# Performance work log

Hardware: AMD Instinct MI355X
Metric: run time of the kernel (lower is better)

## Reference

```python
import jax, jax.numpy as jnp
import numpy as np

BN_INV = 1.0 / np.sqrt(1.0 + 1e-5)  # eval-mode BatchNorm1d with running_mean=0, running_var=1


def _lin_bn_relu(x, W, g, b):
    # Linear(no bias) -> BN(eval) -> ReLU
    return jax.nn.relu((x @ W.T) * (g * BN_INV) + b)


def setup_inputs() -> dict:
    key = jax.random.key(0)
    ks = jax.random.split(key, 24)
    B, P, N, C, H, OUT = 8, 1024, 20, 32, 256, 256
    s = 0.05
    inp = {
        "polylines": jax.random.normal(ks[0], (B, P, N, C), dtype=jnp.float32),
        "polylines_mask": jax.random.randint(ks[1], (B, P, N), 0, 2) > 0,
        # pre_mlps: [Lin(C->H,no bias)+BN+ReLU] x2, Lin(H->H, bias)
        "pre_w0": jax.random.normal(ks[2], (H, C), dtype=jnp.float32) * s,
        "pre_g0": jnp.ones((H,), jnp.float32),
        "pre_b0": jnp.zeros((H,), jnp.float32),
        "pre_w1": jax.random.normal(ks[3], (H, H), dtype=jnp.float32) * s,
        "pre_g1": jnp.ones((H,), jnp.float32),
        "pre_b1": jnp.zeros((H,), jnp.float32),
        "pre_w2": jax.random.normal(ks[4], (H, H), dtype=jnp.float32) * s,
        "pre_bias2": jnp.zeros((H,), jnp.float32),
        # mlps: c_in=2H -> [H,H,H]
        "mlp_w0": jax.random.normal(ks[5], (H, 2 * H), dtype=jnp.float32) * s,
        "mlp_g0": jnp.ones((H,), jnp.float32),
        "mlp_b0": jnp.zeros((H,), jnp.float32),
        "mlp_w1": jax.random.normal(ks[6], (H, H), dtype=jnp.float32) * s,
        "mlp_g1": jnp.ones((H,), jnp.float32),
        "mlp_b1": jnp.zeros((H,), jnp.float32),
        "mlp_w2": jax.random.normal(ks[7], (H, H), dtype=jnp.float32) * s,
        "mlp_bias2": jnp.zeros((H,), jnp.float32),
        # out_mlps (without_norm): Lin(H->H,bias)+ReLU, Lin(H->OUT,bias)
        "out_w0": jax.random.normal(ks[8], (H, H), dtype=jnp.float32) * s,
        "out_b0": jnp.zeros((H,), jnp.float32),
        "out_w1": jax.random.normal(ks[9], (OUT, H), dtype=jnp.float32) * s,
        "out_b1": jnp.zeros((OUT,), jnp.float32),
    }
    return inp


def reference(polylines, polylines_mask,
              pre_w0, pre_g0, pre_b0, pre_w1, pre_g1, pre_b1, pre_w2, pre_bias2,
              mlp_w0, mlp_g0, mlp_b0, mlp_w1, mlp_g1, mlp_b1, mlp_w2, mlp_bias2,
              out_w0, out_b0, out_w1, out_b1):
    # gather->MLP->zero-scatter is equivalent to dense MLP followed by mask-zeroing
    # (all per-point ops are elementwise / last-dim matmuls).
    m = polylines_mask[..., None].astype(polylines.dtype)  # (B,P,N,1)

    x = _lin_bn_relu(polylines, pre_w0, pre_g0, pre_b0)
    x = _lin_bn_relu(x, pre_w1, pre_g1, pre_b1)
    x = (x @ pre_w2.T + pre_bias2) * m                      # (B,P,N,H) zero at invalid

    pooled = x.max(axis=2)                                  # (B,P,H) max over zero-filled buffer
    x = jnp.concatenate(
        [x, jnp.broadcast_to(pooled[:, :, None, :], x.shape)], axis=-1)  # (B,P,N,2H)

    x = _lin_bn_relu(x, mlp_w0, mlp_g0, mlp_b0)
    x = _lin_bn_relu(x, mlp_w1, mlp_g1, mlp_b1)
    x = (x @ mlp_w2.T + mlp_bias2) * m                      # (B,P,N,H)

    buf = x.max(axis=2)                                     # (B,P,H)

    valid = jnp.any(polylines_mask, axis=-1)                # sum(mask)>0
    y = jax.nn.relu(buf @ out_w0.T + out_b0)
    y = (y @ out_w1.T + out_b1) * valid[..., None].astype(buf.dtype)  # (B,P,OUT)
    return y
```

## Files before the change

### kernel.cpp

```cpp
#include <hip/hip_runtime.h>
#include <stdint.h>
#include <stddef.h>

typedef __bf16 bf16;
typedef __bf16 bf16x4 __attribute__((ext_vector_type(4)));
typedef __bf16 bf16x8 __attribute__((ext_vector_type(8)));
typedef float f32x4 __attribute__((ext_vector_type(4)));
typedef float f32x16 __attribute__((ext_vector_type(16)));

#define BNI 0.9999950000374996f
#define NROW 240
#define TOTROW 163840
#define NPOLY 8192

#define AADDR(r, ch) ((r)*256 + ((((ch) ^ ((r)&31)))<<3))

#define OFF_ACT 0
#define OFF_WB  122880
#define OFF_T2  155648
#define OFF_VAL 161792
#define LDS_TOTAL 161840

#define WS_PRE_W0 0
#define WS_PRE_W1 8192
#define WS_PRE_W2 73728
#define WS_MLP_W0 139264
#define WS_MLP_W1 270336
#define WS_MLP_W2 335872
#define WS_OUT_W0 401408
#define WS_OUT_W1 466944

__device__ __forceinline__ bf16 f2b(float f){
  unsigned int i = __builtin_bit_cast(unsigned int, f);
  unsigned int r = i + 0x7fffu + ((i >> 16) & 1u);
  unsigned short h = (unsigned short)(r >> 16);
  return __builtin_bit_cast(bf16, h);
}
__device__ __forceinline__ float b2f(bf16 x){
  unsigned short u = __builtin_bit_cast(unsigned short, x);
  union { unsigned int i; float f; } v; v.i = ((unsigned int)u) << 16; return v.f;
}
__device__ __forceinline__ bf16x8 ld8f(const float* p, float sc){
  f32x4 a = *(const f32x4*)p;
  f32x4 b = *(const f32x4*)(p + 4);
  bf16x8 r;
  #pragma unroll
  for (int j = 0; j < 4; ++j){ r[j] = f2b(a[j]*sc); r[4+j] = f2b(b[j]*sc); }
  return r;
}

__global__ __launch_bounds__(256)
void prep_kernel(const float* s0, const float* s1, const float* s2, const float* s3,
                 const float* s4, const float* s5, const float* s6, const float* s7,
                 const float* g0, const float* g1, const float* g3, const float* g4,
                 bf16* dst)
{
  const int offs[8] = {WS_PRE_W0, WS_PRE_W1, WS_PRE_W2, WS_MLP_W0,
                       WS_MLP_W1, WS_MLP_W2, WS_OUT_W0, WS_OUT_W1};
  const int sz[8]   = {8192, 65536, 65536, 131072, 65536, 65536, 65536, 65536};
  const int ld[8]   = {32, 256, 256, 512, 256, 256, 256, 256};
  int r = blockIdx.y;
  const float* src = s0;
  if (r == 1) src = s1; else if (r == 2) src = s2; else if (r == 3) src = s3;
  else if (r == 4) src = s4; else if (r == 5) src = s5; else if (r == 6) src = s6;
  else if (r == 7) src = s7;
  const float* gp = (r==0)?g0:(r==1)?g1:(r==3)?g3:(r==4)?g4:nullptr;
  int i = (blockIdx.x*256 + threadIdx.x)*8;
  if (i < sz[r]){
    float sc = gp ? gp[i/ld[r]]*BNI : 1.0f;
    *(bf16x8*)&dst[offs[r] + i] = ld8f(src + i, sc);
  }
}

__device__ __forceinline__ void stageLoad(bf16x8* v, const bf16* W, int ldK, int c64, int tid){
  #pragma unroll
  for (int i = 0; i < 8; ++i){
    int id = tid + 256*i;
    int fr = id >> 5, kc = id & 31;
    v[i] = *(const bf16x8*)(W + (size_t)(c64*64 + fr)*ldK + kc*8);
  }
}
__device__ __forceinline__ void stageStore(const bf16x8* v, bf16* wbuf, int tid){
  #pragma unroll
  for (int i = 0; i < 8; ++i){
    int id = tid + 256*i;
    int fr = id >> 5, kc = id & 31;
    *(bf16x8*)&wbuf[fr*256 + ((kc ^ (fr & 31))<<3)] = v[i];
  }
}

template<int RELU, int MASK, int ADDT2>
__device__ __forceinline__ void epiT(
    const f32x16& acc, int nt, int row, int poly, float mk, bool valid,
    bf16* sAct, const bf16* sT2, const float* bptr, int hi)
{
  #pragma unroll
  for (int q2 = 0; q2 < 4; ++q2){
    int f0 = nt*32 + 8*q2 + 4*hi;
    f32x4 bb = *(const f32x4*)(bptr + f0);
    bf16x4 tv = {};
    if (ADDT2) tv = *(const bf16x4*)&sT2[poly*256 + f0];
    bf16x4 o;
    #pragma unroll
    for (int j = 0; j < 4; ++j){
      float v = acc[4*q2 + j];
      if (ADDT2) v += b2f(tv[j]);
      v += bb[j];
      if (RELU) v = fmaxf(v, 0.0f);
      if (MASK) v *= mk;
      o[j] = f2b(v);
    }
    if (valid)
      *(bf16x4*)&sAct[row*256 + (((nt*4 + q2) ^ (row & 31))<<3) + 4*hi] = o;
  }
}

template<int RELU, int MASK, int ADDT2>
__device__ __forceinline__ void layerT(
    bf16* sAct, bf16* wbuf, const bf16* sT2,
    const bf16* W, int ldK, const float* bptr,
    const int* maskp, int blk, int w, int lane32, int hi, int tid)
{
  const int row0 = w*64 + lane32, row1 = w*64 + 32 + lane32;
  bf16x8 B0[16], B1[16];
  #pragma unroll
  for (int t = 0; t < 16; ++t){
    B0[t] = *(const bf16x8*)&sAct[AADDR(row0, 2*t + hi)];
    B1[t] = *(const bf16x8*)&sAct[AADDR(row1, 2*t + hi)];
  }
  float mk0 = 1.0f, mk1 = 1.0f;
  if (MASK){
    int g0 = blk*NROW + row0;
    mk0 = (g0 < TOTROW && maskp[g0]) ? 1.0f : 0.0f;
    int g1 = blk*NROW + row1;
    mk1 = (row1 < NROW && g1 < TOTROW && maskp[g1]) ? 1.0f : 0.0f;
  }
  const int poly0 = row0/20;
  const int poly1 = (row1 < NROW ? row1 : 0)/20;

  bf16x8 st[8];
  stageLoad(st, W, ldK, 0, tid);
  __syncthreads();
  stageStore(st, wbuf, tid);
  #pragma unroll 1
  for (int c = 0; c < 4; ++c){
    __syncthreads();
    if (c < 3) stageLoad(st, W, ldK, c + 1, tid);
    #pragma unroll
    for (int h2 = 0; h2 < 2; ++h2){
      int nt = c*2 + h2;
      f32x16 a0 = {}, a1 = {};
      #pragma unroll
      for (int t = 0; t < 16; ++t){
        int fr = h2*32 + lane32;
        bf16x8 wf = *(const bf16x8*)&wbuf[fr*256 + (((2*t + hi) ^ (fr & 31))<<3)];
        a0 = __builtin_amdgcn_mfma_f32_32x32x16_bf16(wf, B0[t], a0, 0, 0, 0);
        a1 = __builtin_amdgcn_mfma_f32_32x32x16_bf16(wf, B1[t], a1, 0, 0, 0);
      }
      epiT<RELU,MASK,ADDT2>(a0, nt, row0, poly0, mk0, true, sAct, sT2, bptr, hi);
      epiT<RELU,MASK,ADDT2>(a1, nt, row1, poly1, mk1, row1 < NROW, sAct, sT2, bptr, hi);
    }
    if (c < 3){ __syncthreads(); stageStore(st, wbuf, tid); }
  }
}

__device__ __forceinline__ void poolT(const bf16* sAct, bf16* sPool, int tid){
  #pragma unroll
  for (int i = 0; i < 2; ++i){
    int id = tid + 256*i;
    if (id < 384){
      int poly = id >> 5, c = id & 31;
      float m[8];
      bf16x8 v0 = *(const bf16x8*)&sAct[AADDR(poly*20, c)];
      #pragma unroll
      for (int j = 0; j < 8; ++j) m[j] = b2f(v0[j]);
      for (int r = 1; r < 20; ++r){
        bf16x8 v = *(const bf16x8*)&sAct[AADDR(poly*20 + r, c)];
        #pragma unroll
        for (int j = 0; j < 8; ++j) m[j] = fmaxf(m[j], b2f(v[j]));
      }
      bf16x8 o;
      #pragma unroll
      for (int j = 0; j < 8; ++j) o[j] = f2b(m[j]);
      *(bf16x8*)&sPool[AADDR(poly, c)] = o;
    }
  }
}

__global__ __launch_bounds__(256, 1)
void traj_kernel(const float* __restrict__ poly, const int* __restrict__ maskp,
                 const float* pre_b0, const float* pre_b1, const float* pre_bias2,
                 const float* mlp_b0, const float* mlp_b1, const float* mlp_bias2,
                 const float* out_b0, const float* out_b1,
                 const bf16* __restrict__ ws,
                 float* __restrict__ outp)
{
  extern __shared__ char smem[];
  bf16*  sAct   = (bf16*)(smem + OFF_ACT);
  bf16*  wbuf   = (bf16*)(smem + OFF_WB);
  bf16*  sPool  = wbuf;
  bf16*  sT2    = (bf16*)(smem + OFF_T2);
  float* sValid = (float*)(smem + OFF_VAL);
  bf16*  sY     = sAct;

  const int tid = threadIdx.x;
  const int w = tid >> 6, L = tid & 63, lane32 = L & 31, hi = L >> 5;
  const int row0 = w*64 + lane32, row1 = w*64 + 32 + lane32;
  const int blk = blockIdx.x;

  const bf16* pw0 = ws + WS_PRE_W0;
  const bf16* pw1 = ws + WS_PRE_W1;
  const bf16* pw2 = ws + WS_PRE_W2;
  const bf16* mw0 = ws + WS_MLP_W0;
  const bf16* mw1 = ws + WS_MLP_W1;
  const bf16* mw2 = ws + WS_MLP_W2;
  const bf16* ow0 = ws + WS_OUT_W0;
  const bf16* ow1 = ws + WS_OUT_W1;

  #pragma unroll
  for (int i = 0; i < 4; ++i){
    int id = tid + 256*i;
    if (id < 960){
      int row = id >> 2, c = id & 3;
      int grow = blk*NROW + row;
      bf16x8 v = {};
      if (grow < TOTROW) v = ld8f(poly + (size_t)grow*32 + c*8, 1.0f);
      *(bf16x8*)&sAct[AADDR(row, c)] = v;
    }
  }
  if (tid < 12){
    float v = 0.0f;
    #pragma unroll
    for (int r = 0; r < 20; ++r){
      int g = blk*NROW + tid*20 + r;
      if (g < TOTROW && maskp[g]) v = 1.0f;
    }
    sValid[tid] = v;
  }
  __syncthreads();

  {
    bf16x8 Bp0[2], Bp1[2];
    #pragma unroll
    for (int t = 0; t < 2; ++t){
      Bp0[t] = *(const bf16x8*)&sAct[AADDR(row0, 2*t + hi)];
      Bp1[t] = *(const bf16x8*)&sAct[AADDR(row1, 2*t + hi)];
    }
    #pragma unroll 1
    for (int nt = 0; nt < 8; ++nt){
      f32x16 a0 = {}, a1 = {};
      #pragma unroll
      for (int t = 0; t < 2; ++t){
        bf16x8 wf = *(const bf16x8*)(pw0 + (size_t)(nt*32 + lane32)*32 + 16*t + 8*hi);
        a0 = __builtin_amdgcn_mfma_f32_32x32x16_bf16(wf, Bp0[t], a0, 0, 0, 0);
        a1 = __builtin_amdgcn_mfma_f32_32x32x16_bf16(wf, Bp1[t], a1, 0, 0, 0);
      }
      epiT<1,0,0>(a0, nt, row0, 0, 1.0f, true, sAct, sT2, pre_b0, hi);
      epiT<1,0,0>(a1, nt, row1, 0, 1.0f, row1 < NROW, sAct, sT2, pre_b0, hi);
    }
  }

  layerT<1,0,0>(sAct, wbuf, sT2, pw1, 256, pre_b1,    maskp, blk, w, lane32, hi, tid);
  layerT<0,1,0>(sAct, wbuf, sT2, pw2, 256, pre_bias2, maskp, blk, w, lane32, hi, tid);

  __syncthreads();
  poolT(sAct, sPool, tid);
  __syncthreads();

  {
    bf16x8 Bp[16];
    #pragma unroll
    for (int t = 0; t < 16; ++t)
      Bp[t] = *(const bf16x8*)&sPool[AADDR(lane32, 2*t + hi)];
    #pragma unroll 1
    for (int m = 0; m < 2; ++m){
      int nt = w*2 + m;
      f32x16 acc = {};
      #pragma unroll
      for (int t = 0; t < 16; ++t){
        bf16x8 wf = *(const bf16x8*)(mw0 + (size_t)(nt*32 + lane32)*512 + 256 + 16*t + 8*hi);
        acc = __builtin_amdgcn_mfma_f32_32x32x16_bf16(wf, Bp[t], acc, 0, 0, 0);
      }
      if (lane32 < 12){
        #pragma unroll
        for (int q2 = 0; q2 < 4; ++q2){
          int f0 = nt*32 + 8*q2 + 4*hi;
          bf16x4 o;
          #pragma unroll
          for (int j = 0; j < 4; ++j) o[j] = f2b(acc[4*q2 + j]);
          *(bf16x4*)&sT2[lane32*256 + f0] = o;
        }
      }
    }
  }
  __syncthreads();

  layerT<1,0,1>(sAct, wbuf, sT2, mw0, 512, mlp_b0,    maskp, blk, w, lane32, hi, tid);
  layerT<1,0,0>(sAct, wbuf, sT2, mw1, 256, mlp_b1,    maskp, blk, w, lane32, hi, tid);
  layerT<0,1,0>(sAct, wbuf, sT2, mw2, 256, mlp_bias2, maskp, blk, w, lane32, hi, tid);

  __syncthreads();
  poolT(sAct, sPool, tid);
  __syncthreads();

  {
    bf16x8 Bp[16];
    #pragma unroll
    for (int t = 0; t < 16; ++t)
      Bp[t] = *(const bf16x8*)&sPool[AADDR(lane32, 2*t + hi)];
    #pragma unroll 1
    for (int m = 0; m < 2; ++m){
      int nt = w*2 + m;
      f32x16 acc = {};
      #pragma unroll
      for (int t = 0; t < 16; ++t){
        bf16x8 wf = *(const bf16x8*)(ow0 + (size_t)(nt*32 + lane32)*256 + 16*t + 8*hi);
        acc = __builtin_amdgcn_mfma_f32_32x32x16_bf16(wf, Bp[t], acc, 0, 0, 0);
      }
      if (lane32 < 12){
        #pragma unroll
        for (int q2 = 0; q2 < 4; ++q2){
          int f0 = nt*32 + 8*q2 + 4*hi;
          f32x4 bb = *(const f32x4*)(out_b0 + f0);
          bf16x4 o;
          #pragma unroll
          for (int j = 0; j < 4; ++j) o[j] = f2b(fmaxf(acc[4*q2 + j] + bb[j], 0.0f));
          *(bf16x4*)&sY[lane32*256 + (((nt*4 + q2) ^ (lane32 & 31))<<3) + 4*hi] = o;
        }
      }
    }
  }
  __syncthreads();

  {
    bf16x8 By[16];
    #pragma unroll
    for (int t = 0; t < 16; ++t)
      By[t] = *(const bf16x8*)&sY[AADDR(lane32, 2*t + hi)];
    #pragma unroll 1
    for (int m = 0; m < 2; ++m){
      int nt = w*2 + m;
      f32x16 acc = {};
      #pragma unroll
      for (int t = 0; t < 16; ++t){
        bf16x8 wf = *(const bf16x8*)(ow1 + (size_t)(nt*32 + lane32)*256 + 16*t + 8*hi);
        acc = __builtin_amdgcn_mfma_f32_32x32x16_bf16(wf, By[t], acc, 0, 0, 0);
      }
      int gp = blk*12 + lane32;
      if (lane32 < 12 && gp < NPOLY){
        float vd = sValid[lane32];
        #pragma unroll
        for (int q2 = 0; q2 < 4; ++q2){
          int f0 = nt*32 + 8*q2 + 4*hi;
          f32x4 bb = *(const f32x4*)(out_b1 + f0);
          f32x4 o;
          #pragma unroll
          for (int j = 0; j < 4; ++j) o[j] = (acc[4*q2 + j] + bb[j]) * vd;
          *(f32x4*)&outp[(size_t)gp*256 + f0] = o;
        }
      }
    }
  }
}

extern "C" void kernel_launch(void* const* d_in, const int* in_sizes, int n_in,
                              void* d_out, int out_size, void* d_ws, size_t ws_size,
                              hipStream_t stream)
{
  const float* poly      = (const float*)d_in[0];
  const int*   maskp     = (const int*)  d_in[1];
  const float* pre_w0    = (const float*)d_in[2];
  const float* pre_g0    = (const float*)d_in[3];
  const float* pre_b0    = (const float*)d_in[4];
  const float* pre_w1    = (const float*)d_in[5];
  const float* pre_g1    = (const float*)d_in[6];
  const float* pre_b1    = (const float*)d_in[7];
  const float* pre_w2    = (const float*)d_in[8];
  const float* pre_bias2 = (const float*)d_in[9];
  const float* mlp_w0    = (const float*)d_in[10];
  const float* mlp_g0    = (const float*)d_in[11];
  const float* mlp_b0    = (const float*)d_in[12];
  const float* mlp_w1    = (const float*)d_in[13];
  const float* mlp_g1    = (const float*)d_in[14];
  const float* mlp_b1    = (const float*)d_in[15];
  const float* mlp_w2    = (const float*)d_in[16];
  const float* mlp_bias2 = (const float*)d_in[17];
  const float* out_w0    = (const float*)d_in[18];
  const float* out_b0    = (const float*)d_in[19];
  const float* out_w1    = (const float*)d_in[20];
  const float* out_b1    = (const float*)d_in[21];

  bf16* ws = (bf16*)d_ws;

  (void)hipFuncSetAttribute((const void*)&traj_kernel,
                            hipFuncAttributeMaxDynamicSharedMemorySize, LDS_TOTAL);

  prep_kernel<<<dim3(64, 8), dim3(256), 0, stream>>>(
      pre_w0, pre_w1, pre_w2, mlp_w0, mlp_w1, mlp_w2, out_w0, out_w1,
      pre_g0, pre_g1, mlp_g0, mlp_g1, ws);

  traj_kernel<<<dim3(683), dim3(256), LDS_TOTAL, stream>>>(
      poly, maskp,
      pre_b0, pre_b1, pre_bias2,
      mlp_b0, mlp_b1, mlp_bias2,
      out_b0, out_b1,
      ws, (float*)d_out);
}
```

Baseline: 362.6 us.

## Use 512-thread blocks with one row tile per wave and global weight loads

```diff
diff --git a/kernel.cpp b/kernel.cpp
--- a/kernel.cpp
+++ b/kernel.cpp
@@ -15,11 +15,11 @@
 
 #define AADDR(r, ch) ((r)*256 + ((((ch) ^ ((r)&31)))<<3))
 
-#define OFF_ACT 0
-#define OFF_WB  122880
-#define OFF_T2  155648
-#define OFF_VAL 161792
-#define LDS_TOTAL 161840
+#define OFF_ACT  0
+#define OFF_POOL 122880
+#define OFF_T2   139264
+#define OFF_VAL  145408
+#define LDS_TOTAL 145456
 
 #define WS_PRE_W0 0
 #define WS_PRE_W1 8192
@@ -72,23 +72,6 @@
   }
 }
 
-__device__ __forceinline__ void stageLoad(bf16x8* v, const bf16* W, int ldK, int c64, int tid){
-  #pragma unroll
-  for (int i = 0; i < 8; ++i){
-    int id = tid + 256*i;
-    int fr = id >> 5, kc = id & 31;
-    v[i] = *(const bf16x8*)(W + (size_t)(c64*64 + fr)*ldK + kc*8);
-  }
-}
-__device__ __forceinline__ void stageStore(const bf16x8* v, bf16* wbuf, int tid){
-  #pragma unroll
-  for (int i = 0; i < 8; ++i){
-    int id = tid + 256*i;
-    int fr = id >> 5, kc = id & 31;
-    *(bf16x8*)&wbuf[fr*256 + ((kc ^ (fr & 31))<<3)] = v[i];
-  }
-}
-
 template<int RELU, int MASK, int ADDT2>
 __device__ __forceinline__ void epiT(
     const f32x16& acc, int nt, int row, int poly, float mk, bool valid,
@@ -117,77 +100,57 @@
 
 template<int RELU, int MASK, int ADDT2>
 __device__ __forceinline__ void layerT(
-    bf16* sAct, bf16* wbuf, const bf16* sT2,
+    bf16* sAct, const bf16* sT2,
     const bf16* W, int ldK, const float* bptr,
-    const int* maskp, int blk, int w, int lane32, int hi, int tid)
-{
-  const int row0 = w*64 + lane32, row1 = w*64 + 32 + lane32;
-  bf16x8 B0[16], B1[16];
+    const int* maskp, int blk, int row, int rowc, int lane32, int hi)
+{
+  bf16x8 B[16];
   #pragma unroll
-  for (int t = 0; t < 16; ++t){
-    B0[t] = *(const bf16x8*)&sAct[AADDR(row0, 2*t + hi)];
-    B1[t] = *(const bf16x8*)&sAct[AADDR(row1, 2*t + hi)];
-  }
-  float mk0 = 1.0f, mk1 = 1.0f;
+  for (int t = 0; t < 16; ++t)
+    B[t] = *(const bf16x8*)&sAct[AADDR(rowc, 2*t + hi)];
+
+  float mk = 1.0f;
   if (MASK){
-    int g0 = blk*NROW + row0;
-    mk0 = (g0 < TOTROW && maskp[g0]) ? 1.0f : 0.0f;
-    int g1 = blk*NROW + row1;
-    mk1 = (row1 < NROW && g1 < TOTROW && maskp[g1]) ? 1.0f : 0.0f;
-  }
-  const int poly0 = row0/20;
-  const int poly1 = (row1 < NROW ? row1 : 0)/20;
-
-  bf16x8 st[8];
-  stageLoad(st, W, ldK, 0, tid);
-  __syncthreads();
-  stageStore(st, wbuf, tid);
+    int g = blk*NROW + row;
+    mk = (row < NROW && g < TOTROW && maskp[g]) ? 1.0f : 0.0f;
+  }
+  const int poly = rowc/20;
+  const bool valid = row < NROW;
+
   #pragma unroll 1
-  for (int c = 0; c < 4; ++c){
-    __syncthreads();
-    if (c < 3) stageLoad(st, W, ldK, c + 1, tid);
-    #pragma unroll
-    for (int h2 = 0; h2 < 2; ++h2){
-      int nt = c*2 + h2;
-      f32x16 a0 = {}, a1 = {};
+  for (int nt = 0; nt < 8; ++nt){
+    const bf16* p = W + (size_t)(nt*32 + lane32)*ldK + 8*hi;
+    bf16x8 wf[16];
+    #pragma unroll
+    for (int t = 0; t < 16; ++t) wf[t] = *(const bf16x8*)(p + 16*t);
+    f32x16 acc = {};
+    #pragma unroll
+    for (int t = 0; t < 16; ++t)
+      acc = __builtin_amdgcn_mfma_f32_32x32x16_bf16(wf[t], B[t], acc, 0, 0, 0);
+    epiT<RELU,MASK,ADDT2>(acc, nt, row, poly, mk, valid, sAct, sT2, bptr, hi);
+  }
+}
+
+__device__ __forceinline__ void poolT(const bf16* sAct, bf16* sPool, int tid){
+  if (tid < 384){
+    int poly = tid >> 5, c = tid & 31;
+    float m[8];
+    bf16x8 v0 = *(const bf16x8*)&sAct[AADDR(poly*20, c)];
+    #pragma unroll
+    for (int j = 0; j < 8; ++j) m[j] = b2f(v0[j]);
+    for (int r = 1; r < 20; ++r){
+      bf16x8 v = *(const bf16x8*)&sAct[AADDR(poly*20 + r, c)];
       #pragma unroll
-      for (int t = 0; t < 16; ++t){
-        int fr = h2*32 + lane32;
-        bf16x8 wf = *(const bf16x8*)&wbuf[fr*256 + (((2*t + hi) ^ (fr & 31))<<3)];
-        a0 = __builtin_amdgcn_mfma_f32_32x32x16_bf16(wf, B0[t], a0, 0, 0, 0);
-        a1 = __builtin_amdgcn_mfma_f32_32x32x16_bf16(wf, B1[t], a1, 0, 0, 0);
-      }
-      epiT<RELU,MASK,ADDT2>(a0, nt, row0, poly0, mk0, true, sAct, sT2, bptr, hi);
-      epiT<RELU,MASK,ADDT2>(a1, nt, row1, poly1, mk1, row1 < NROW, sAct, sT2, bptr, hi);
-    }
-    if (c < 3){ __syncthreads(); stageStore(st, wbuf, tid); }
-  }
-}
-
-__device__ __forceinline__ void poolT(const bf16* sAct, bf16* sPool, int tid){
-  #pragma unroll
-  for (int i = 0; i < 2; ++i){
-    int id = tid + 256*i;
-    if (id < 384){
-      int poly = id >> 5, c = id & 31;
-      float m[8];
-      bf16x8 v0 = *(const bf16x8*)&sAct[AADDR(poly*20, c)];
-      #pragma unroll
-      for (int j = 0; j < 8; ++j) m[j] = b2f(v0[j]);
-      for (int r = 1; r < 20; ++r){
-        bf16x8 v = *(const bf16x8*)&sAct[AADDR(poly*20 + r, c)];
-        #pragma unroll
-        for (int j = 0; j < 8; ++j) m[j] = fmaxf(m[j], b2f(v[j]));
-      }
-      bf16x8 o;
-      #pragma unroll
-      for (int j = 0; j < 8; ++j) o[j] = f2b(m[j]);
-      *(bf16x8*)&sPool[AADDR(poly, c)] = o;
-    }
-  }
-}
-
-__global__ __launch_bounds__(256, 1)
+      for (int j = 0; j < 8; ++j) m[j] = fmaxf(m[j], b2f(v[j]));
+    }
+    bf16x8 o;
+    #pragma unroll
+    for (int j = 0; j < 8; ++j) o[j] = f2b(m[j]);
+    *(bf16x8*)&sPool[AADDR(poly, c)] = o;
+  }
+}
+
+__global__ __launch_bounds__(512, 2)
 void traj_kernel(const float* __restrict__ poly, const int* __restrict__ maskp,
                  const float* pre_b0, const float* pre_b1, const float* pre_bias2,
                  const float* mlp_b0, const float* mlp_b1, const float* mlp_bias2,
@@ -197,15 +160,15 @@
 {
   extern __shared__ char smem[];
   bf16*  sAct   = (bf16*)(smem + OFF_ACT);
-  bf16*  wbuf   = (bf16*)(smem + OFF_WB);
-  bf16*  sPool  = wbuf;
+  bf16*  sPool  = (bf16*)(smem + OFF_POOL);
   bf16*  sT2    = (bf16*)(smem + OFF_T2);
   float* sValid = (float*)(smem + OFF_VAL);
   bf16*  sY     = sAct;
 
   const int tid = threadIdx.x;
   const int w = tid >> 6, L = tid & 63, lane32 = L & 31, hi = L >> 5;
-  const int row0 = w*64 + lane32, row1 = w*64 + 32 + lane32;
+  const int row  = w*32 + lane32;
+  const int rowc = row < NROW ? row : NROW - 1;
   const int blk = blockIdx.x;
 
   const bf16* pw0 = ws + WS_PRE_W0;
@@ -218,16 +181,17 @@
   const bf16* ow1 = ws + WS_OUT_W1;
 
   #pragma unroll
-  for (int i = 0; i < 4; ++i){
-    int id = tid + 256*i;
+  for (int i = 0; i < 2; ++i){
+    int id = tid + 512*i;
     if (id < 960){
-      int row = id >> 2, c = id & 3;
-      int grow = blk*NROW + row;
+      int r = id >> 2, c = id & 3;
+      int grow = blk*NROW + r;
       bf16x8 v = {};
       if (grow < TOTROW) v = ld8f(poly + (size_t)grow*32 + c*8, 1.0f);
-      *(bf16x8*)&sAct[AADDR(row, c)] = v;
-    }
-  }
+      *(bf16x8*)&sAct[AADDR(r, c)] = v;
+    }
+  }
+  __syncthreads();
   if (tid < 12){
     float v = 0.0f;
     #pragma unroll
@@ -237,31 +201,24 @@
     }
     sValid[tid] = v;
   }
-  __syncthreads();
 
   {
-    bf16x8 Bp0[2], Bp1[2];
-    #pragma unroll
-    for (int t = 0; t < 2; ++t){
-      Bp0[t] = *(const bf16x8*)&sAct[AADDR(row0, 2*t + hi)];
-      Bp1[t] = *(const bf16x8*)&sAct[AADDR(row1, 2*t + hi)];
-    }
+    bf16x8 B0 = *(const bf16x8*)&sAct[AADDR(rowc, hi)];
+    bf16x8 B1 = *(const bf16x8*)&sAct[AADDR(rowc, 2 + hi)];
     #pragma unroll 1
     for (int nt = 0; nt < 8; ++nt){
-      f32x16 a0 = {}, a1 = {};
-      #pragma unroll
-      for (int t = 0; t < 2; ++t){
-        bf16x8 wf = *(const bf16x8*)(pw0 + (size_t)(nt*32 + lane32)*32 + 16*t + 8*hi);
-        a0 = __builtin_amdgcn_mfma_f32_32x32x16_bf16(wf, Bp0[t], a0, 0, 0, 0);
-        a1 = __builtin_amdgcn_mfma_f32_32x32x16_bf16(wf, Bp1[t], a1, 0, 0, 0);
-      }
-      epiT<1,0,0>(a0, nt, row0, 0, 1.0f, true, sAct, sT2, pre_b0, hi);
-      epiT<1,0,0>(a1, nt, row1, 0, 1.0f, row1 < NROW, sAct, sT2, pre_b0, hi);
-    }
-  }
-
-  layerT<1,0,0>(sAct, wbuf, sT2, pw1, 256, pre_b1,    maskp, blk, w, lane32, hi, tid);
-  layerT<0,1,0>(sAct, wbuf, sT2, pw2, 256, pre_bias2, maskp, blk, w, lane32, hi, tid);
+      const bf16* p = pw0 + (size_t)(nt*32 + lane32)*32 + 8*hi;
+      bf16x8 w0 = *(const bf16x8*)p;
+      bf16x8 w1 = *(const bf16x8*)(p + 16);
+      f32x16 acc = {};
+      acc = __builtin_amdgcn_mfma_f32_32x32x16_bf16(w0, B0, acc, 0, 0, 0);
+      acc = __builtin_amdgcn_mfma_f32_32x32x16_bf16(w1, B1, acc, 0, 0, 0);
+      epiT<1,0,0>(acc, nt, row, 0, 1.0f, row < NROW, sAct, sT2, pre_b0, hi);
+    }
+  }
+
+  layerT<1,0,0>(sAct, sT2, pw1, 256, pre_b1,    maskp, blk, row, rowc, lane32, hi);
+  layerT<0,1,0>(sAct, sT2, pw2, 256, pre_bias2, maskp, blk, row, rowc, lane32, hi);
 
   __syncthreads();
   poolT(sAct, sPool, tid);
@@ -271,33 +228,31 @@
     bf16x8 Bp[16];
     #pragma unroll
     for (int t = 0; t < 16; ++t)
-      Bp[t] = *(const bf16x8*)&sPool[AADDR(lane32, 2*t + hi)];
-    #pragma unroll 1
-    for (int m = 0; m < 2; ++m){
-      int nt = w*2 + m;
-      f32x16 acc = {};
+      Bp[t] = *(const bf16x8*)&sPool[AADDR((lane32 < 12 ? lane32 : 0), 2*t + hi)];
+    int nt = w;
+    const bf16* p = mw0 + (size_t)(nt*32 + lane32)*512 + 256 + 8*hi;
+    f32x16 acc = {};
+    #pragma unroll
+    for (int t = 0; t < 16; ++t){
+      bf16x8 wf = *(const bf16x8*)(p + 16*t);
+      acc = __builtin_amdgcn_mfma_f32_32x32x16_bf16(wf, Bp[t], acc, 0, 0, 0);
+    }
+    if (lane32 < 12){
       #pragma unroll
-      for (int t = 0; t < 16; ++t){
-        bf16x8 wf = *(const bf16x8*)(mw0 + (size_t)(nt*32 + lane32)*512 + 256 + 16*t + 8*hi);
-        acc = __builtin_amdgcn_mfma_f32_32x32x16_bf16(wf, Bp[t], acc, 0, 0, 0);
+      for (int q2 = 0; q2 < 4; ++q2){
+        int f0 = nt*32 + 8*q2 + 4*hi;
+        bf16x4 o;
+        #pragma unroll
+        for (int j = 0; j < 4; ++j) o[j] = f2b(acc[4*q2 + j]);
+        *(bf16x4*)&sT2[lane32*256 + f0] = o;
       }
-      if (lane32 < 12){
-        #pragma unroll
-        for (int q2 = 0; q2 < 4; ++q2){
-          int f0 = nt*32 + 8*q2 + 4*hi;
-          bf16x4 o;
-          #pragma unroll
-          for (int j = 0; j < 4; ++j) o[j] = f2b(acc[4*q2 + j]);
-          *(bf16x4*)&sT2[lane32*256 + f0] = o;
-        }
-      }
-    }
-  }
-  __syncthreads();
-
-  layerT<1,0,1>(sAct, wbuf, sT2, mw0, 512, mlp_b0,    maskp, blk, w, lane32, hi, tid);
-  layerT<1,0,0>(sAct, wbuf, sT2, mw1, 256, mlp_b1,    maskp, blk, w, lane32, hi, tid);
-  layerT<0,1,0>(sAct, wbuf, sT2, mw2, 256, mlp_bias2, maskp, blk, w, lane32, hi, tid);
+    }
+  }
+  __syncthreads();
+
+  layerT<1,0,1>(sAct, sT2, mw0, 512, mlp_b0,    maskp, blk, row, rowc, lane32, hi);
+  layerT<1,0,0>(sAct, sT2, mw1, 256, mlp_b1,    maskp, blk, row, rowc, lane32, hi);
+  layerT<0,1,0>(sAct, sT2, mw2, 256, mlp_bias2, maskp, blk, row, rowc, lane32, hi);
 
   __syncthreads();
   poolT(sAct, sPool, tid);
@@ -307,26 +262,24 @@
     bf16x8 Bp[16];
     #pragma unroll
     for (int t = 0; t < 16; ++t)
-      Bp[t] = *(const bf16x8*)&sPool[AADDR(lane32, 2*t + hi)];
-    #pragma unroll 1
-    for (int m = 0; m < 2; ++m){
-      int nt = w*2 + m;
-      f32x16 acc = {};
+      Bp[t] = *(const bf16x8*)&sPool[AADDR((lane32 < 12 ? lane32 : 0), 2*t + hi)];
+    int nt = w;
+    const bf16* p = ow0 + (size_t)(nt*32 + lane32)*256 + 8*hi;
+    f32x16 acc = {};
+    #pragma unroll
+    for (int t = 0; t < 16; ++t){
+      bf16x8 wf = *(const bf16x8*)(p + 16*t);
+      acc = __builtin_amdgcn_mfma_f32_32x32x16_bf16(wf, Bp[t], acc, 0, 0, 0);
+    }
+    if (lane32 < 12){
       #pragma unroll
-      for (int t = 0; t < 16; ++t){
-        bf16x8 wf = *(const bf16x8*)(ow0 + (size_t)(nt*32 + lane32)*256 + 16*t + 8*hi);
-        acc = __builtin_amdgcn_mfma_f32_32x32x16_bf16(wf, Bp[t], acc, 0, 0, 0);
-      }
-      if (lane32 < 12){
+      for (int q2 = 0; q2 < 4; ++q2){
+        int f0 = nt*32 + 8*q2 + 4*hi;
+        f32x4 bb = *(const f32x4*)(out_b0 + f0);
+        bf16x4 o;
         #pragma unroll
-        for (int q2 = 0; q2 < 4; ++q2){
-          int f0 = nt*32 + 8*q2 + 4*hi;
-          f32x4 bb = *(const f32x4*)(out_b0 + f0);
-          bf16x4 o;
-          #pragma unroll
-          for (int j = 0; j < 4; ++j) o[j] = f2b(fmaxf(acc[4*q2 + j] + bb[j], 0.0f));
-          *(bf16x4*)&sY[lane32*256 + (((nt*4 + q2) ^ (lane32 & 31))<<3) + 4*hi] = o;
-        }
+        for (int j = 0; j < 4; ++j) o[j] = f2b(fmaxf(acc[4*q2 + j] + bb[j], 0.0f));
+        *(bf16x4*)&sY[lane32*256 + (((nt*4 + q2) ^ (lane32 & 31))<<3) + 4*hi] = o;
       }
     }
   }
@@ -336,28 +289,26 @@
     bf16x8 By[16];
     #pragma unroll
     for (int t = 0; t < 16; ++t)
-      By[t] = *(const bf16x8*)&sY[AADDR(lane32, 2*t + hi)];
-    #pragma unroll 1
-    for (int m = 0; m < 2; ++m){
-      int nt = w*2 + m;
-      f32x16 acc = {};
+      By[t] = *(const bf16x8*)&sY[AADDR((lane32 < 12 ? lane32 : 0), 2*t + hi)];
+    int nt = w;
+    const bf16* p = ow1 + (size_t)(nt*32 + lane32)*256 + 8*hi;
+    f32x16 acc = {};
+    #pragma unroll
+    for (int t = 0; t < 16; ++t){
+      bf16x8 wf = *(const bf16x8*)(p + 16*t);
+      acc = __builtin_amdgcn_mfma_f32_32x32x16_bf16(wf, By[t], acc, 0, 0, 0);
+    }
+    int gp = blk*12 + lane32;
+    if (lane32 < 12 && gp < NPOLY){
+      float vd = sValid[lane32];
       #pragma unroll
-      for (int t = 0; t < 16; ++t){
-        bf16x8 wf = *(const bf16x8*)(ow1 + (size_t)(nt*32 + lane32)*256 + 16*t + 8*hi);
-        acc = __builtin_amdgcn_mfma_f32_32x32x16_bf16(wf, By[t], acc, 0, 0, 0);
-      }
-      int gp = blk*12 + lane32;
-      if (lane32 < 12 && gp < NPOLY){
-        float vd = sValid[lane32];
+      for (int q2 = 0; q2 < 4; ++q2){
+        int f0 = nt*32 + 8*q2 + 4*hi;
+        f32x4 bb = *(const f32x4*)(out_b1 + f0);
+        f32x4 o;
         #pragma unroll
-        for (int q2 = 0; q2 < 4; ++q2){
-          int f0 = nt*32 + 8*q2 + 4*hi;
-          f32x4 bb = *(const f32x4*)(out_b1 + f0);
-          f32x4 o;
-          #pragma unroll
-          for (int j = 0; j < 4; ++j) o[j] = (acc[4*q2 + j] + bb[j]) * vd;
-          *(f32x4*)&outp[(size_t)gp*256 + f0] = o;
-        }
+        for (int j = 0; j < 4; ++j) o[j] = (acc[4*q2 + j] + bb[j]) * vd;
+        *(f32x4*)&outp[(size_t)gp*256 + f0] = o;
       }
     }
   }
@@ -399,7 +350,7 @@
       pre_w0, pre_w1, pre_w2, mlp_w0, mlp_w1, mlp_w2, out_w0, out_w1,
       pre_g0, pre_g1, mlp_g0, mlp_g1, ws);
 
-  traj_kernel<<<dim3(683), dim3(256), LDS_TOTAL, stream>>>(
+  traj_kernel<<<dim3(683), dim3(512), LDS_TOTAL, stream>>>(
       poly, maskp,
       pre_b0, pre_b1, pre_bias2,
       mlp_b0, mlp_b1, mlp_bias2,
```

Result: slower. 628.5 us (+73.3%).
